# Kernel optimization log

Hardware: AMD Instinct MI355X
Metric: run time of the kernel (lower is better)

Reference implementation:

```python
import jax, jax.numpy as jnp
import numpy as np

D = 256  # subgraph_width
N_CLASSES = 10
EPS = 1e-5  # torch LayerNorm default


def _layernorm(x, g, b):
    mu = jnp.mean(x, axis=-1, keepdims=True)
    var = jnp.var(x, axis=-1, keepdims=True)
    return (x - mu) * jax.lax.rsqrt(var + EPS) * g + b


def setup_inputs() -> dict:
    key = jax.random.key(0)
    ks = jax.random.split(key, 16)
    B, T, N = 64, 512, 512
    traj = jax.random.normal(ks[0], (B, T, 2), dtype=jnp.float32)
    labels = jax.random.randint(ks[1], (B,), 0, N_CLASSES)
    h = jax.random.normal(ks[2], (B, N, D), dtype=jnp.float32)
    valid_len = jnp.maximum(jax.random.randint(ks[3], (B,), 0, N), 1)
    s = 0.02
    params = dict(
        emb=jax.random.normal(ks[4], (N_CLASSES, D), dtype=jnp.float32) * s,
        w_mlp=jax.random.normal(ks[5], (2, D), dtype=jnp.float32) * s,
        b_mlp=jnp.zeros((D,), jnp.float32),
        ln_g=jnp.ones((D,), jnp.float32),
        ln_b=jnp.zeros((D,), jnp.float32),
        wq=jax.random.normal(ks[6], (D, D), dtype=jnp.float32) * s,
        bq=jnp.zeros((D,), jnp.float32),
        wk=jax.random.normal(ks[7], (D, D), dtype=jnp.float32) * s,
        bk=jnp.zeros((D,), jnp.float32),
        wv=jax.random.normal(ks[8], (D, D), dtype=jnp.float32) * s,
        bv=jnp.zeros((D,), jnp.float32),
        w_out=jax.random.normal(ks[9], (D, 1), dtype=jnp.float32) * s,
        b_out=jnp.zeros((1,), jnp.float32),
    )
    return dict(traj=traj, labels=labels, h=h, valid_len=valid_len, **params)


def reference(traj, labels, h, valid_len, emb, w_mlp, b_mlp, ln_g, ln_b,
              wq, bq, wk, bk, wv, bv, w_out, b_out):
    # MLP(in=2, out=D, activation='leaky'): Linear -> LayerNorm -> LeakyReLU
    x = jax.nn.leaky_relu(_layernorm(traj @ w_mlp + b_mlp, ln_g, ln_b))  # [B,T,D]
    le = emb[labels]                          # [B,D]
    x = x + le[:, None, :]                    # embed-add
    # SelfAttentionWithKeyFCLayer: Q from x, K/V from h, scaled, key-masked by valid_len
    q = x @ wq + bq                            # [B,T,D]
    k = h @ wk + bk                            # [B,N,D]
    v = h @ wv + bv                            # [B,N,D]
    scores = jnp.einsum('btd,bnd->btn', q, k) / jnp.sqrt(jnp.float32(D))
    N = h.shape[1]
    key_mask = jnp.arange(N)[None, :] < valid_len[:, None]          # [B,N]
    scores = jnp.where(key_mask[:, None, :], scores, jnp.float32(-1e9))
    attn = jax.nn.softmax(scores, axis=-1)
    enc = jnp.einsum('btn,bnd->btd', attn, v)  # [B,T,D]
    pooled = jnp.max(enc, axis=1) + le          # [B,D]
    return jax.nn.sigmoid(pooled @ w_out + b_out)  # [B,1]
```

## Files before the change

kernel.cpp:

```cpp
#include <hip/hip_runtime.h>
#include <math.h>

typedef float f32x4 __attribute__((ext_vector_type(4)));
typedef __bf16 bf16x8 __attribute__((ext_vector_type(8)));
typedef unsigned short u16x8 __attribute__((ext_vector_type(8)));
typedef unsigned short u16x4 __attribute__((ext_vector_type(4)));
typedef unsigned int u32x4 __attribute__((ext_vector_type(4)));

#define MFMA(a, b, c) __builtin_amdgcn_mfma_f32_16x16x32_bf16((a), (b), (c), 0, 0, 0)

static __device__ __forceinline__ unsigned short f2bf(float f) {
  unsigned u = __float_as_uint(f);
  u += 0x7FFFu + ((u >> 16) & 1u);
  return (unsigned short)(u >> 16);
}
static __device__ __forceinline__ float bf2f(unsigned short s) {
  return __uint_as_float(((unsigned)s) << 16);
}
static __device__ __forceinline__ unsigned pack2bf(float lo, float hi) {
  return (unsigned)f2bf(lo) | ((unsigned)f2bf(hi) << 16);
}

static __device__ __forceinline__ int swz512(int row, int col) {
  return row * 512 + (col ^ ((((row & 7) ^ (col >> 6)) & 7) << 4));
}
static __device__ __forceinline__ int swzV(int d, int col) {
  return d * 64 + (col ^ (((d >> 1) & 3) << 4));
}
static __device__ __forceinline__ int swzO(int d, int col) {
  return d * 256 + (col ^ ((((d & 7) ^ (col >> 7)) & 7) << 4));
}

__global__ __launch_bounds__(256) void setup(
    const float* __restrict__ w0m, const float* __restrict__ w1m, const float* __restrict__ w2m,
    unsigned short* __restrict__ t0m, unsigned short* __restrict__ t1m, unsigned short* __restrict__ t2m,
    const float* __restrict__ w_mlp, const float* __restrict__ b_mlp, float* __restrict__ lnsc,
    const int* __restrict__ vlen, int* __restrict__ tasktab) {
  int bid = blockIdx.x;
  int t = threadIdx.x;
  if (bid == 48) {
    float w0 = w_mlp[t], w1 = w_mlp[256 + t], bb = b_mlp[t];
    float v[9] = {w0, w1, bb, w0 * w0, w1 * w1, w0 * w1, w0 * bb, w1 * bb, bb * bb};
    __shared__ float red[4][9];
#pragma unroll
    for (int j = 0; j < 9; ++j) {
      float s = v[j];
#pragma unroll
      for (int off = 32; off >= 1; off >>= 1) s += __shfl_xor(s, off, 64);
      v[j] = s;
    }
    if ((t & 63) == 0)
      for (int j = 0; j < 9; ++j) red[t >> 6][j] = v[j];
    __syncthreads();
    if (t < 9) lnsc[t] = red[0][t] + red[1][t] + red[2][t] + red[3][t];
    return;
  }
  if (bid == 49) {
    __shared__ int srank[64];
    if (t < 64) {
      int vb = vlen[t], r = 0;
      for (int j = 0; j < 64; ++j) {
        int vj = vlen[j];
        r += (vj > vb) || (vj == vb && j < t);
      }
      srank[r] = t;
    }
    __syncthreads();
    if (t < 64) {
      int r = t, b = srank[r];
      int xcd = r & 7, a = r >> 3;
      for (int tt = 0; tt < 4; ++tt)
        tasktab[(a * 4 + tt) * 8 + xcd] = (b << 2) | tt;
    }
    return;
  }
  int m = bid >> 4, t16 = bid & 15;
  const float* w = (m == 0) ? w0m : (m == 1) ? w1m : w2m;
  unsigned short* o = (m == 0) ? t0m : (m == 1) ? t1m : t2m;
  __shared__ float sm[64][65];
  int bi = t16 >> 2, bj = t16 & 3;
  for (int kb = 0; kb < 16; ++kb) {
    int idx = kb * 256 + t;
    int r = idx >> 6, c = idx & 63;
    sm[r][c] = w[(bi * 64 + r) * 256 + bj * 64 + c];
  }
  __syncthreads();
  for (int kb = 0; kb < 16; ++kb) {
    int idx = kb * 256 + t;
    int r = idx >> 6, c = idx & 63;
    int d = bj * 64 + r, e = bi * 64 + c;
    o[(e >> 5) * 8192 + d * 32 + (e & 31)] = f2bf(sm[c][r]);
  }
}

static __device__ __forceinline__ void gemm_direct(
    const unsigned short* __restrict__ Bpk, const unsigned short* Alds,
    int w, int g, int c15, f32x4 (&acc)[4][4]) {
  const unsigned short* bp = Bpk + (w * 64 + c15) * 32 + 8 * g;
#pragma unroll
  for (int c = 0; c < 8; ++c) {
    bf16x8 bfv[4];
#pragma unroll
    for (int nt = 0; nt < 4; ++nt)
      bfv[nt] = *(const bf16x8*)(bp + c * 8192 + nt * 512);
    bf16x8 af[4];
#pragma unroll
    for (int at = 0; at < 4; ++at)
      af[at] = *(const bf16x8*)((char*)Alds + swz512(at * 16 + c15, c * 64 + 16 * g));
    __builtin_amdgcn_s_setprio(1);
#pragma unroll
    for (int at = 0; at < 4; ++at)
#pragma unroll
      for (int nt = 0; nt < 4; ++nt) acc[at][nt] = MFMA(af[at], bfv[nt], acc[at][nt]);
    __builtin_amdgcn_s_setprio(0);
  }
}

__global__ __launch_bounds__(256, 4) void gemms(
    const float* __restrict__ h, const int* __restrict__ vlen,
    const unsigned short* __restrict__ wkPk, const float* __restrict__ bk,
    const unsigned short* __restrict__ wvPk, const float* __restrict__ bv,
    unsigned short* __restrict__ kout, unsigned short* __restrict__ vT) {
  __shared__ unsigned short Alds[64 * 256];
  int tid = threadIdx.x, w = tid >> 6, lane = tid & 63, g = lane >> 4, c15 = lane & 15;
  int tile = blockIdx.x;
  int b = tile >> 3;
  int nbase = (tile & 7) * 64;
  if (nbase >= vlen[b]) return;
  f32x4 acc[4][4];
  {
    const float* hb = h + (size_t)tile * 16384;
    f32x4 ha[8], hc[8];
#pragma unroll
    for (int i = 0; i < 8; ++i) {
      ha[i] = *(const f32x4*)(hb + i * 2048 + tid * 8);
      hc[i] = *(const f32x4*)(hb + i * 2048 + tid * 8 + 4);
    }
#pragma unroll
    for (int i = 0; i < 8; ++i) {
      u16x8 pk;
#pragma unroll
      for (int j = 0; j < 4; ++j) { pk[j] = f2bf(ha[i][j]); pk[j + 4] = f2bf(hc[i][j]); }
      *(u16x8*)((char*)Alds + swz512(i * 8 + (tid >> 5), (tid & 31) * 16)) = pk;
    }
  }
#pragma unroll
  for (int a = 0; a < 4; ++a)
#pragma unroll
    for (int n = 0; n < 4; ++n) acc[a][n] = (f32x4){0.f, 0.f, 0.f, 0.f};
  __syncthreads();

  gemm_direct(wvPk, Alds, w, g, c15, acc);
#pragma unroll
  for (int at = 0; at < 4; ++at)
#pragma unroll
    for (int nt = 0; nt < 4; ++nt) {
      int col = w * 64 + nt * 16 + c15;
      float bb = bv[col];
      u16x4 o;
#pragma unroll
      for (int r = 0; r < 4; ++r) o[r] = f2bf(acc[at][nt][r] + bb);
      *(u16x4*)(vT + (size_t)b * 131072 + (size_t)col * 512 + nbase + at * 16 + 4 * g) = o;
    }

#pragma unroll
  for (int a = 0; a < 4; ++a)
#pragma unroll
    for (int n = 0; n < 4; ++n) acc[a][n] = (f32x4){0.f, 0.f, 0.f, 0.f};
  gemm_direct(wkPk, Alds, w, g, c15, acc);
  __syncthreads();
#pragma unroll
  for (int at = 0; at < 4; ++at)
#pragma unroll
    for (int nt = 0; nt < 4; ++nt) {
      int col = w * 64 + nt * 16 + c15;
      float bb = bk[col];
#pragma unroll
      for (int r = 0; r < 4; ++r)
        *(unsigned short*)((char*)Alds + swz512(at * 16 + 4 * g + r, col * 2)) =
            f2bf(acc[at][nt][r] + bb);
    }
  __syncthreads();
  {
    int row = tid >> 2;
    for (int i = 0; i < 8; ++i) {
      int colb = (tid & 3) * 128 + i * 16;
      u16x8 vv = *(const u16x8*)((char*)Alds + swz512(row, colb));
      *(u16x8*)(kout + (size_t)(tile * 64 + row) * 256 + colb / 2) = vv;
    }
  }
}

__global__ __launch_bounds__(512, 2) void attn(
    const float* __restrict__ traj, const int* __restrict__ labels,
    const float* __restrict__ emb, const float* __restrict__ w_mlp,
    const float* __restrict__ b_mlp, const float* __restrict__ ln_g,
    const float* __restrict__ ln_b, const float* __restrict__ lnsc,
    const unsigned short* __restrict__ wqPk, const float* __restrict__ bq,
    const unsigned short* __restrict__ k, const unsigned short* __restrict__ vT,
    const int* __restrict__ valid_len, const int* __restrict__ tasktab,
    float* __restrict__ partial) {
  __shared__ unsigned short buf[2][16384];

  int task = tasktab[blockIdx.x];
  int b = task >> 2, tt = task & 3;
  int tid = threadIdx.x, w = tid >> 6, lane = tid & 63, g = lane >> 4, c15 = lane & 15;
  int vl = valid_len[b];
  int nit = (vl + 31) >> 5;
  bool isA = (w < 4);
  int wq4 = w & 3;

  {
    int rrow = tid >> 5, cb = (tid & 31) * 8;
    int lab = labels[b];
    f32x4 wa0 = *(const f32x4*)(w_mlp + cb), wa1 = *(const f32x4*)(w_mlp + cb + 4);
    f32x4 wb0 = *(const f32x4*)(w_mlp + 256 + cb), wb1 = *(const f32x4*)(w_mlp + 256 + cb + 4);
    f32x4 bm0 = *(const f32x4*)(b_mlp + cb), bm1 = *(const f32x4*)(b_mlp + cb + 4);
    f32x4 g0 = *(const f32x4*)(ln_g + cb), g1 = *(const f32x4*)(ln_g + cb + 4);
    f32x4 lb0 = *(const f32x4*)(ln_b + cb), lb1 = *(const f32x4*)(ln_b + cb + 4);
    f32x4 le0 = *(const f32x4*)(emb + lab * 256 + cb), le1 = *(const f32x4*)(emb + lab * 256 + cb + 4);
    float s0 = lnsc[0], s1 = lnsc[1], s2 = lnsc[2], s3 = lnsc[3], s4 = lnsc[4],
          s5 = lnsc[5], s6 = lnsc[6], s7 = lnsc[7], s8 = lnsc[8];
#pragma unroll
    for (int i = 0; i < 8; ++i) {
      int row = i * 16 + rrow, grow = b * 512 + tt * 128 + row;
      float t0 = traj[grow * 2], t1 = traj[grow * 2 + 1];
      float mu = (t0 * s0 + t1 * s1 + s2) * (1.f / 256.f);
      float ea2 = (t0 * t0 * s3 + t1 * t1 * s4 + s8 +
                   2.f * (t0 * t1 * s5 + t0 * s6 + t1 * s7)) * (1.f / 256.f);
      float rstd = rsqrtf(ea2 - mu * mu + 1e-5f);
      u16x8 pk;
#pragma unroll
      for (int j = 0; j < 4; ++j) {
        float a0 = t0 * wa0[j] + t1 * wb0[j] + bm0[j];
        float y0 = (a0 - mu) * rstd * g0[j] + lb0[j];
        pk[j] = f2bf((y0 > 0.f ? y0 : 0.01f * y0) + le0[j]);
        float a1 = t0 * wa1[j] + t1 * wb1[j] + bm1[j];
        float y1 = (a1 - mu) * rstd * g1[j] + lb1[j];
        pk[j + 4] = f2bf((y1 > 0.f ? y1 : 0.01f * y1) + le1[j]);
      }
      *(u16x8*)((char*)buf + swz512(row, cb * 2)) = pk;
    }
  }
  __syncthreads();

  {
    f32x4 qacc[4][4];
#pragma unroll
    for (int a = 0; a < 4; ++a)
#pragma unroll
      for (int n = 0; n < 4; ++n) qacc[a][n] = (f32x4){0.f, 0.f, 0.f, 0.f};
    int rbase = (w >> 2) * 64;
    const unsigned short* bp = wqPk + (wq4 * 64 + c15) * 32 + 8 * g;
#pragma unroll
    for (int c = 0; c < 8; ++c) {
      bf16x8 bfv[4];
#pragma unroll
      for (int nt = 0; nt < 4; ++nt)
        bfv[nt] = *(const bf16x8*)(bp + c * 8192 + nt * 512);
      bf16x8 af[4];
#pragma unroll
      for (int at = 0; at < 4; ++at)
        af[at] = *(const bf16x8*)((char*)buf + swz512(rbase + at * 16 + c15, c * 64 + 16 * g));
      __builtin_amdgcn_s_setprio(1);
#pragma unroll
      for (int at = 0; at < 4; ++at)
#pragma unroll
        for (int nt = 0; nt < 4; ++nt) qacc[at][nt] = MFMA(af[at], bfv[nt], qacc[at][nt]);
      __builtin_amdgcn_s_setprio(0);
    }
    __syncthreads();
#pragma unroll
    for (int nt = 0; nt < 4; ++nt) {
      int col = wq4 * 64 + nt * 16 + c15;
      float bb = bq[col];
#pragma unroll
      for (int at = 0; at < 4; ++at)
#pragma unroll
        for (int r = 0; r < 4; ++r)
          *(unsigned short*)((char*)buf + swz512(rbase + at * 16 + 4 * g + r, col * 2)) =
              f2bf(qacc[at][nt][r] + bb);
    }
  }
  __syncthreads();
  bf16x8 qf[2][8];
  if (isA) {
#pragma unroll
    for (int qt = 0; qt < 2; ++qt)
#pragma unroll
      for (int kk = 0; kk < 8; ++kk)
        qf[qt][kk] = *(const bf16x8*)((char*)buf + swz512(qt * 64 + wq4 * 16 + c15, kk * 64 + 16 * g));
  }
  __syncthreads();

  f32x4 acco[2][16];
#pragma unroll
  for (int qt = 0; qt < 2; ++qt)
#pragma unroll
    for (int i = 0; i < 16; ++i) acco[qt][i] = (f32x4){0.f, 0.f, 0.f, 0.f};
  float rs[2] = {0.f, 0.f};

  const unsigned short* kbase = k + (size_t)b * 512 * 256;
  const unsigned short* vbase = vT + (size_t)b * 131072;
  int t2 = tid & 255;

  if (!isA) {
    u16x8 kp[4], vp[4];
#pragma unroll
    for (int i = 0; i < 4; ++i) {
      int idx = t2 + 256 * i, key = idx >> 5, s = idx & 31;
      kp[i] = *(const u16x8*)(kbase + (size_t)key * 256 + s * 8);
    }
#pragma unroll
    for (int i = 0; i < 4; ++i) {
      int idx = t2 + 256 * i, d = idx >> 2, s = idx & 3;
      vp[i] = *(const u16x8*)(vbase + (size_t)d * 512 + s * 8);
    }
#pragma unroll
    for (int i = 0; i < 4; ++i) {
      int idx = t2 + 256 * i, key = idx >> 5, s = idx & 31;
      *(u16x8*)((char*)buf[0] + swz512(key, s * 16)) = kp[i];
    }
#pragma unroll
    for (int i = 0; i < 4; ++i) {
      int idx = t2 + 256 * i, d = idx >> 2, s = idx & 3;
      *(u16x8*)((char*)(buf[0] + 8192) + swzV(d, s * 16)) = vp[i];
    }
  }

  for (int it = 0; it < nit; ++it) {
    __syncthreads();
    if (isA) {
      const unsigned short* Klds = buf[it & 1];
      const unsigned short* Vlds = buf[it & 1] + 8192;
      int n0 = it * 32;
      f32x4 s4[2][2];
#pragma unroll
      for (int qt = 0; qt < 2; ++qt)
#pragma unroll
        for (int c = 0; c < 2; ++c) s4[qt][c] = (f32x4){0.f, 0.f, 0.f, 0.f};
      __builtin_amdgcn_s_setprio(1);
#pragma unroll
      for (int c = 0; c < 2; ++c)
#pragma unroll
        for (int kk = 0; kk < 8; ++kk) {
          bf16x8 kf = *(const bf16x8*)((char*)Klds + swz512(c * 16 + c15, kk * 64 + 16 * g));
          s4[0][c] = MFMA(kf, qf[0][kk], s4[0][c]);
          s4[1][c] = MFMA(kf, qf[1][kk], s4[1][c]);
        }
      __builtin_amdgcn_s_setprio(0);
      unsigned u01[2][2], u23[2][2];
#pragma unroll
      for (int qt = 0; qt < 2; ++qt)
#pragma unroll
        for (int c = 0; c < 2; ++c) {
          float p4[4];
#pragma unroll
          for (int r = 0; r < 4; ++r) {
            int key = n0 + c * 16 + 4 * g + r;
            float pv = (key < vl) ? __expf(s4[qt][c][r] * 0.0625f) : 0.f;
            p4[r] = pv;
            rs[qt] += pv;
          }
          u01[qt][c] = pack2bf(p4[0], p4[1]);
          u23[qt][c] = pack2bf(p4[2], p4[3]);
        }
      int srcA = c15 | ((lane & 16) << 1);
      int srcB = srcA + 16;
      bool hi = g >= 2;
      union { u32x4 u; bf16x8 v; } pa[2];
#pragma unroll
      for (int qt = 0; qt < 2; ++qt) {
        unsigned x0a = (unsigned)__shfl((int)u01[qt][0], srcA, 64);
        unsigned x1a = (unsigned)__shfl((int)u01[qt][1], srcA, 64);
        unsigned x0b = (unsigned)__shfl((int)u23[qt][0], srcA, 64);
        unsigned x1b = (unsigned)__shfl((int)u23[qt][1], srcA, 64);
        unsigned x0c = (unsigned)__shfl((int)u01[qt][0], srcB, 64);
        unsigned x1c = (unsigned)__shfl((int)u01[qt][1], srcB, 64);
        unsigned x0d = (unsigned)__shfl((int)u23[qt][0], srcB, 64);
        unsigned x1d = (unsigned)__shfl((int)u23[qt][1], srcB, 64);
        pa[qt].u[0] = hi ? x1a : x0a;
        pa[qt].u[1] = hi ? x1b : x0b;
        pa[qt].u[2] = hi ? x1c : x0c;
        pa[qt].u[3] = hi ? x1d : x0d;
      }
      __builtin_amdgcn_s_setprio(1);
#pragma unroll
      for (int dt = 0; dt < 16; ++dt) {
        bf16x8 vf = *(const bf16x8*)((char*)Vlds + swzV(dt * 16 + c15, 16 * g));
        acco[0][dt] = MFMA(vf, pa[0].v, acco[0][dt]);
        acco[1][dt] = MFMA(vf, pa[1].v, acco[1][dt]);
      }
      __builtin_amdgcn_s_setprio(0);
    } else if (it + 1 < nit) {
      int n1 = (it + 1) * 32;
      unsigned short* Kn = buf[(it + 1) & 1];
      unsigned short* Vn = buf[(it + 1) & 1] + 8192;
      u16x8 kp[4], vp[4];
#pragma unroll
      for (int i = 0; i < 4; ++i) {
        int idx = t2 + 256 * i, key = idx >> 5, s = idx & 31;
        kp[i] = *(const u16x8*)(kbase + (size_t)(n1 + key) * 256 + s * 8);
      }
#pragma unroll
      for (int i = 0; i < 4; ++i) {
        int idx = t2 + 256 * i, d = idx >> 2, s = idx & 3;
        vp[i] = *(const u16x8*)(vbase + (size_t)d * 512 + n1 + s * 8);
      }
#pragma unroll
      for (int i = 0; i < 4; ++i) {
        int idx = t2 + 256 * i, key = idx >> 5, s = idx & 31;
        *(u16x8*)((char*)Kn + swz512(key, s * 16)) = kp[i];
      }
#pragma unroll
      for (int i = 0; i < 4; ++i) {
        int idx = t2 + 256 * i, d = idx >> 2, s = idx & 3;
        *(u16x8*)((char*)Vn + swzV(d, s * 16)) = vp[i];
      }
    }
  }

  float inv[2];
  if (isA) {
#pragma unroll
    for (int qt = 0; qt < 2; ++qt) {
      rs[qt] += __shfl_xor(rs[qt], 16, 64);
      rs[qt] += __shfl_xor(rs[qt], 32, 64);
      inv[qt] = 1.f / rs[qt];
    }
  }
  __syncthreads();
  if (isA) {
#pragma unroll
    for (int qt = 0; qt < 2; ++qt) {
      int qcol = qt * 64 + wq4 * 16 + c15;
#pragma unroll
      for (int dt = 0; dt < 16; ++dt)
#pragma unroll
        for (int r = 0; r < 4; ++r) {
          int d = dt * 16 + 4 * g + r;
          *(unsigned short*)((char*)buf + swzO(d, qcol * 2)) = f2bf(acco[qt][dt][r] * inv[qt]);
        }
    }
  }
  __syncthreads();
  {
    int d = tid & 255, half = tid >> 8;
    float m = -1e30f;
    for (int i = 0; i < 8; ++i) {
      u16x8 vv = *(const u16x8*)((char*)buf + swzO(d, half * 128 + i * 16));
#pragma unroll
      for (int j = 0; j < 8; ++j) m = fmaxf(m, bf2f(vv[j]));
    }
    partial[(((size_t)b * 4 + tt) * 2 + half) * 256 + d] = m;
  }
}

__global__ __launch_bounds__(256) void finalize(
    const float* __restrict__ partial, const float* __restrict__ emb,
    const int* __restrict__ labels, const float* __restrict__ w_out,
    const float* __restrict__ b_out, float* __restrict__ out) {
  int b = blockIdx.x, t = threadIdx.x;
  float m = -1e30f;
#pragma unroll
  for (int s8 = 0; s8 < 8; ++s8)
    m = fmaxf(m, partial[((size_t)b * 8 + s8) * 256 + t]);
  m += emb[labels[b] * 256 + t];
  __shared__ float red[256];
  red[t] = m * w_out[t];
  __syncthreads();
  for (int s = 128; s > 0; s >>= 1) {
    if (t < s) red[t] += red[t + s];
    __syncthreads();
  }
  if (t == 0) out[b] = 1.f / (1.f + __expf(-(red[0] + b_out[0])));
}

extern "C" void kernel_launch(void* const* d_in, const int* in_sizes, int n_in,
                              void* d_out, int out_size, void* d_ws, size_t ws_size,
                              hipStream_t stream) {
  const float* traj   = (const float*)d_in[0];
  const int*   labels = (const int*)d_in[1];
  const float* h      = (const float*)d_in[2];
  const int*   vlen   = (const int*)d_in[3];
  const float* emb    = (const float*)d_in[4];
  const float* w_mlp  = (const float*)d_in[5];
  const float* b_mlp  = (const float*)d_in[6];
  const float* ln_g   = (const float*)d_in[7];
  const float* ln_b   = (const float*)d_in[8];
  const float* wq     = (const float*)d_in[9];
  const float* bq     = (const float*)d_in[10];
  const float* wk     = (const float*)d_in[11];
  const float* bk     = (const float*)d_in[12];
  const float* wv     = (const float*)d_in[13];
  const float* bv     = (const float*)d_in[14];
  const float* w_out  = (const float*)d_in[15];
  const float* b_out  = (const float*)d_in[16];
  float* out = (float*)d_out;

  unsigned short* kb   = (unsigned short*)d_ws;
  unsigned short* vT   = kb + (size_t)32768 * 256;
  unsigned short* wqPk = vT + (size_t)32768 * 256;
  unsigned short* wkPk = wqPk + 65536;
  unsigned short* wvPk = wkPk + 65536;
  float* lnsc    = (float*)(wvPk + 65536);
  float* partial = lnsc + 16;
  int*   tasktab = (int*)(partial + 64 * 8 * 256);

  setup<<<50, 256, 0, stream>>>(wq, wk, wv, wqPk, wkPk, wvPk, w_mlp, b_mlp, lnsc,
                                vlen, tasktab);
  gemms<<<512, 256, 0, stream>>>(h, vlen, wkPk, bk, wvPk, bv, kb, vT);
  attn<<<256, 512, 0, stream>>>(traj, labels, emb, w_mlp, b_mlp, ln_g, ln_b, lnsc,
                                wqPk, bq, kb, vT, vlen, tasktab, partial);
  finalize<<<64, 256, 0, stream>>>(partial, emb, labels, w_out, b_out, out);
}
```

Measured before the change: 79.06 us.

## Split attention into 64-row tasks and run K/V gemms on separate waves

Result: slower. 112.5 us (+42.3%).

```diff
diff --git a/kernel.cpp b/kernel.cpp
--- a/kernel.cpp
+++ b/kernel.cpp
@@ -27,8 +27,8 @@
 static __device__ __forceinline__ int swzV(int d, int col) {
   return d * 64 + (col ^ (((d >> 1) & 3) << 4));
 }
-static __device__ __forceinline__ int swzO(int d, int col) {
-  return d * 256 + (col ^ ((((d & 7) ^ (col >> 7)) & 7) << 4));
+static __device__ __forceinline__ int swzO64(int d, int col) {
+  return d * 128 + (col ^ ((d & 7) << 4));
 }
 
 __global__ __launch_bounds__(256) void setup(
@@ -69,8 +69,8 @@
     if (t < 64) {
       int r = t, b = srank[r];
       int xcd = r & 7, a = r >> 3;
-      for (int tt = 0; tt < 4; ++tt)
-        tasktab[(a * 4 + tt) * 8 + xcd] = (b << 2) | tt;
+      for (int tt = 0; tt < 8; ++tt)
+        tasktab[(a * 8 + tt) * 8 + xcd] = (b << 3) | tt;
     }
     return;
   }
@@ -116,12 +116,13 @@
   }
 }
 
-__global__ __launch_bounds__(256, 4) void gemms(
+__global__ __launch_bounds__(512, 4) void gemms(
     const float* __restrict__ h, const int* __restrict__ vlen,
     const unsigned short* __restrict__ wkPk, const float* __restrict__ bk,
     const unsigned short* __restrict__ wvPk, const float* __restrict__ bv,
     unsigned short* __restrict__ kout, unsigned short* __restrict__ vT) {
   __shared__ unsigned short Alds[64 * 256];
+  __shared__ unsigned short Klds[64 * 256];
   int tid = threadIdx.x, w = tid >> 6, lane = tid & 63, g = lane >> 4, c15 = lane & 15;
   int tile = blockIdx.x;
   int b = tile >> 3;
@@ -130,18 +131,18 @@
   f32x4 acc[4][4];
   {
     const float* hb = h + (size_t)tile * 16384;
-    f32x4 ha[8], hc[8];
-#pragma unroll
-    for (int i = 0; i < 8; ++i) {
-      ha[i] = *(const f32x4*)(hb + i * 2048 + tid * 8);
-      hc[i] = *(const f32x4*)(hb + i * 2048 + tid * 8 + 4);
-    }
-#pragma unroll
-    for (int i = 0; i < 8; ++i) {
+    f32x4 ha[4], hc[4];
+#pragma unroll
+    for (int i = 0; i < 4; ++i) {
+      ha[i] = *(const f32x4*)(hb + i * 4096 + tid * 8);
+      hc[i] = *(const f32x4*)(hb + i * 4096 + tid * 8 + 4);
+    }
+#pragma unroll
+    for (int i = 0; i < 4; ++i) {
       u16x8 pk;
 #pragma unroll
       for (int j = 0; j < 4; ++j) { pk[j] = f2bf(ha[i][j]); pk[j + 4] = f2bf(hc[i][j]); }
-      *(u16x8*)((char*)Alds + swz512(i * 8 + (tid >> 5), (tid & 31) * 16)) = pk;
+      *(u16x8*)((char*)Alds + swz512(i * 16 + (tid >> 5), (tid & 31) * 16)) = pk;
     }
   }
 #pragma unroll
@@ -150,48 +151,46 @@
     for (int n = 0; n < 4; ++n) acc[a][n] = (f32x4){0.f, 0.f, 0.f, 0.f};
   __syncthreads();
 
-  gemm_direct(wvPk, Alds, w, g, c15, acc);
-#pragma unroll
-  for (int at = 0; at < 4; ++at)
-#pragma unroll
-    for (int nt = 0; nt < 4; ++nt) {
-      int col = w * 64 + nt * 16 + c15;
-      float bb = bv[col];
-      u16x4 o;
-#pragma unroll
-      for (int r = 0; r < 4; ++r) o[r] = f2bf(acc[at][nt][r] + bb);
-      *(u16x4*)(vT + (size_t)b * 131072 + (size_t)col * 512 + nbase + at * 16 + 4 * g) = o;
-    }
-
-#pragma unroll
-  for (int a = 0; a < 4; ++a)
-#pragma unroll
-    for (int n = 0; n < 4; ++n) acc[a][n] = (f32x4){0.f, 0.f, 0.f, 0.f};
-  gemm_direct(wkPk, Alds, w, g, c15, acc);
-  __syncthreads();
-#pragma unroll
-  for (int at = 0; at < 4; ++at)
-#pragma unroll
-    for (int nt = 0; nt < 4; ++nt) {
-      int col = w * 64 + nt * 16 + c15;
-      float bb = bk[col];
-#pragma unroll
-      for (int r = 0; r < 4; ++r)
-        *(unsigned short*)((char*)Alds + swz512(at * 16 + 4 * g + r, col * 2)) =
-            f2bf(acc[at][nt][r] + bb);
-    }
-  __syncthreads();
-  {
+  int w4 = w & 3;
+  if (w < 4) {
+    gemm_direct(wvPk, Alds, w4, g, c15, acc);
+#pragma unroll
+    for (int at = 0; at < 4; ++at)
+#pragma unroll
+      for (int nt = 0; nt < 4; ++nt) {
+        int col = w4 * 64 + nt * 16 + c15;
+        float bb = bv[col];
+        u16x4 o;
+#pragma unroll
+        for (int r = 0; r < 4; ++r) o[r] = f2bf(acc[at][nt][r] + bb);
+        *(u16x4*)(vT + (size_t)b * 131072 + (size_t)col * 512 + nbase + at * 16 + 4 * g) = o;
+      }
+  } else {
+    gemm_direct(wkPk, Alds, w4, g, c15, acc);
+#pragma unroll
+    for (int at = 0; at < 4; ++at)
+#pragma unroll
+      for (int nt = 0; nt < 4; ++nt) {
+        int col = w4 * 64 + nt * 16 + c15;
+        float bb = bk[col];
+#pragma unroll
+        for (int r = 0; r < 4; ++r)
+          *(unsigned short*)((char*)Klds + swz512(at * 16 + 4 * g + r, col * 2)) =
+              f2bf(acc[at][nt][r] + bb);
+      }
+  }
+  __syncthreads();
+  if (tid < 256) {
     int row = tid >> 2;
     for (int i = 0; i < 8; ++i) {
       int colb = (tid & 3) * 128 + i * 16;
-      u16x8 vv = *(const u16x8*)((char*)Alds + swz512(row, colb));
+      u16x8 vv = *(const u16x8*)((char*)Klds + swz512(row, colb));
       *(u16x8*)(kout + (size_t)(tile * 64 + row) * 256 + colb / 2) = vv;
     }
   }
 }
 
-__global__ __launch_bounds__(512, 2) void attn(
+__global__ __launch_bounds__(256, 2) void attn(
     const float* __restrict__ traj, const int* __restrict__ labels,
     const float* __restrict__ emb, const float* __restrict__ w_mlp,
     const float* __restrict__ b_mlp, const float* __restrict__ ln_g,
@@ -200,15 +199,16 @@
     const unsigned short* __restrict__ k, const unsigned short* __restrict__ vT,
     const int* __restrict__ valid_len, const int* __restrict__ tasktab,
     float* __restrict__ partial) {
-  __shared__ unsigned short buf[2][16384];
+  __shared__ unsigned short ring[2][16384];
 
   int task = tasktab[blockIdx.x];
-  int b = task >> 2, tt = task & 3;
+  int b = task >> 3, tt = task & 7;
   int tid = threadIdx.x, w = tid >> 6, lane = tid & 63, g = lane >> 4, c15 = lane & 15;
   int vl = valid_len[b];
   int nit = (vl + 31) >> 5;
-  bool isA = (w < 4);
-  int wq4 = w & 3;
+  bool isA = (w < 2);
+  int cw = w & 1;
+  int tp = tid & 127;
 
   {
     int rrow = tid >> 5, cb = (tid & 31) * 8;
@@ -219,14 +219,14 @@
     f32x4 g0 = *(const f32x4*)(ln_g + cb), g1 = *(const f32x4*)(ln_g + cb + 4);
     f32x4 lb0 = *(const f32x4*)(ln_b + cb), lb1 = *(const f32x4*)(ln_b + cb + 4);
     f32x4 le0 = *(const f32x4*)(emb + lab * 256 + cb), le1 = *(const f32x4*)(emb + lab * 256 + cb + 4);
-    float s0 = lnsc[0], s1 = lnsc[1], s2 = lnsc[2], s3 = lnsc[3], s4 = lnsc[4],
+    float s0 = lnsc[0], s1 = lnsc[1], s2 = lnsc[2], s3 = lnsc[3], s4_ = lnsc[4],
           s5 = lnsc[5], s6 = lnsc[6], s7 = lnsc[7], s8 = lnsc[8];
 #pragma unroll
     for (int i = 0; i < 8; ++i) {
-      int row = i * 16 + rrow, grow = b * 512 + tt * 128 + row;
+      int row = i * 8 + rrow, grow = b * 512 + tt * 64 + row;
       float t0 = traj[grow * 2], t1 = traj[grow * 2 + 1];
       float mu = (t0 * s0 + t1 * s1 + s2) * (1.f / 256.f);
-      float ea2 = (t0 * t0 * s3 + t1 * t1 * s4 + s8 +
+      float ea2 = (t0 * t0 * s3 + t1 * t1 * s4_ + s8 +
                    2.f * (t0 * t1 * s5 + t0 * s6 + t1 * s7)) * (1.f / 256.f);
       float rstd = rsqrtf(ea2 - mu * mu + 1e-5f);
       u16x8 pk;
@@ -239,7 +239,7 @@
         float y1 = (a1 - mu) * rstd * g1[j] + lb1[j];
         pk[j + 4] = f2bf((y1 > 0.f ? y1 : 0.01f * y1) + le1[j]);
       }
-      *(u16x8*)((char*)buf + swz512(row, cb * 2)) = pk;
+      *(u16x8*)((char*)ring + swz512(row, cb * 2)) = pk;
     }
   }
   __syncthreads();
@@ -250,89 +250,72 @@
     for (int a = 0; a < 4; ++a)
 #pragma unroll
       for (int n = 0; n < 4; ++n) qacc[a][n] = (f32x4){0.f, 0.f, 0.f, 0.f};
-    int rbase = (w >> 2) * 64;
-    const unsigned short* bp = wqPk + (wq4 * 64 + c15) * 32 + 8 * g;
-#pragma unroll
-    for (int c = 0; c < 8; ++c) {
-      bf16x8 bfv[4];
-#pragma unroll
-      for (int nt = 0; nt < 4; ++nt)
-        bfv[nt] = *(const bf16x8*)(bp + c * 8192 + nt * 512);
-      bf16x8 af[4];
+    gemm_direct(wqPk, (const unsigned short*)ring, w, g, c15, qacc);
+#pragma unroll
+    for (int nt = 0; nt < 4; ++nt) {
+      int col = w * 64 + nt * 16 + c15;
+      float bb = bq[col];
 #pragma unroll
       for (int at = 0; at < 4; ++at)
-        af[at] = *(const bf16x8*)((char*)buf + swz512(rbase + at * 16 + c15, c * 64 + 16 * g));
-      __builtin_amdgcn_s_setprio(1);
-#pragma unroll
-      for (int at = 0; at < 4; ++at)
-#pragma unroll
-        for (int nt = 0; nt < 4; ++nt) qacc[at][nt] = MFMA(af[at], bfv[nt], qacc[at][nt]);
-      __builtin_amdgcn_s_setprio(0);
-    }
-    __syncthreads();
-#pragma unroll
-    for (int nt = 0; nt < 4; ++nt) {
-      int col = wq4 * 64 + nt * 16 + c15;
-      float bb = bq[col];
-#pragma unroll
-      for (int at = 0; at < 4; ++at)
 #pragma unroll
         for (int r = 0; r < 4; ++r)
-          *(unsigned short*)((char*)buf + swz512(rbase + at * 16 + 4 * g + r, col * 2)) =
+          *(unsigned short*)((char*)ring + 32768 + swz512(at * 16 + 4 * g + r, col * 2)) =
               f2bf(qacc[at][nt][r] + bb);
     }
   }
   __syncthreads();
+
+  f32x4 acco[2][16];
+#pragma unroll
+  for (int qt = 0; qt < 2; ++qt)
+#pragma unroll
+    for (int i = 0; i < 16; ++i) acco[qt][i] = (f32x4){0.f, 0.f, 0.f, 0.f};
+  float rs[2] = {0.f, 0.f};
+
+  const unsigned short* kbase = k + (size_t)b * 512 * 256;
+  const unsigned short* vbase = vT + (size_t)b * 131072;
+
+  auto STAGE = [&](int slot, int n0) {
+    char* base = (char*)ring + slot * 32768;
+    u16x8 kp[8], vp[8];
+#pragma unroll
+    for (int i = 0; i < 8; ++i) {
+      int idx = tp + 128 * i, key = idx >> 5, s = idx & 31;
+      kp[i] = *(const u16x8*)(kbase + (size_t)(n0 + key) * 256 + s * 8);
+    }
+#pragma unroll
+    for (int i = 0; i < 8; ++i) {
+      int idx = tp + 128 * i, d = idx >> 2, s = idx & 3;
+      vp[i] = *(const u16x8*)(vbase + (size_t)d * 512 + n0 + s * 8);
+    }
+#pragma unroll
+    for (int i = 0; i < 8; ++i) {
+      int idx = tp + 128 * i, key = idx >> 5, s = idx & 31;
+      *(u16x8*)(base + swz512(key, s * 16)) = kp[i];
+    }
+#pragma unroll
+    for (int i = 0; i < 8; ++i) {
+      int idx = tp + 128 * i, d = idx >> 2, s = idx & 3;
+      *(u16x8*)(base + 16384 + swzV(d, s * 16)) = vp[i];
+    }
+  };
+
   bf16x8 qf[2][8];
   if (isA) {
 #pragma unroll
     for (int qt = 0; qt < 2; ++qt)
 #pragma unroll
       for (int kk = 0; kk < 8; ++kk)
-        qf[qt][kk] = *(const bf16x8*)((char*)buf + swz512(qt * 64 + wq4 * 16 + c15, kk * 64 + 16 * g));
-  }
-  __syncthreads();
-
-  f32x4 acco[2][16];
-#pragma unroll
-  for (int qt = 0; qt < 2; ++qt)
-#pragma unroll
-    for (int i = 0; i < 16; ++i) acco[qt][i] = (f32x4){0.f, 0.f, 0.f, 0.f};
-  float rs[2] = {0.f, 0.f};
-
-  const unsigned short* kbase = k + (size_t)b * 512 * 256;
-  const unsigned short* vbase = vT + (size_t)b * 131072;
-  int t2 = tid & 255;
-
-  if (!isA) {
-    u16x8 kp[4], vp[4];
-#pragma unroll
-    for (int i = 0; i < 4; ++i) {
-      int idx = t2 + 256 * i, key = idx >> 5, s = idx & 31;
-      kp[i] = *(const u16x8*)(kbase + (size_t)key * 256 + s * 8);
-    }
-#pragma unroll
-    for (int i = 0; i < 4; ++i) {
-      int idx = t2 + 256 * i, d = idx >> 2, s = idx & 3;
-      vp[i] = *(const u16x8*)(vbase + (size_t)d * 512 + s * 8);
-    }
-#pragma unroll
-    for (int i = 0; i < 4; ++i) {
-      int idx = t2 + 256 * i, key = idx >> 5, s = idx & 31;
-      *(u16x8*)((char*)buf[0] + swz512(key, s * 16)) = kp[i];
-    }
-#pragma unroll
-    for (int i = 0; i < 4; ++i) {
-      int idx = t2 + 256 * i, d = idx >> 2, s = idx & 3;
-      *(u16x8*)((char*)(buf[0] + 8192) + swzV(d, s * 16)) = vp[i];
-    }
-  }
+        qf[qt][kk] = *(const bf16x8*)((char*)ring + 32768 +
+                                      swz512(cw * 32 + qt * 16 + c15, kk * 64 + 16 * g));
+  } else {
+    STAGE(0, 0);
+  }
+  __syncthreads();
 
   for (int it = 0; it < nit; ++it) {
-    __syncthreads();
     if (isA) {
-      const unsigned short* Klds = buf[it & 1];
-      const unsigned short* Vlds = buf[it & 1] + 8192;
+      const char* base = (const char*)ring + (it & 1) * 32768;
       int n0 = it * 32;
       f32x4 s4[2][2];
 #pragma unroll
@@ -344,7 +327,7 @@
       for (int c = 0; c < 2; ++c)
 #pragma unroll
         for (int kk = 0; kk < 8; ++kk) {
-          bf16x8 kf = *(const bf16x8*)((char*)Klds + swz512(c * 16 + c15, kk * 64 + 16 * g));
+          bf16x8 kf = *(const bf16x8*)(base + swz512(c * 16 + c15, kk * 64 + 16 * g));
           s4[0][c] = MFMA(kf, qf[0][kk], s4[0][c]);
           s4[1][c] = MFMA(kf, qf[1][kk], s4[1][c]);
         }
@@ -387,37 +370,15 @@
       __builtin_amdgcn_s_setprio(1);
 #pragma unroll
       for (int dt = 0; dt < 16; ++dt) {
-        bf16x8 vf = *(const bf16x8*)((char*)Vlds + swzV(dt * 16 + c15, 16 * g));
+        bf16x8 vf = *(const bf16x8*)(base + 16384 + swzV(dt * 16 + c15, 16 * g));
         acco[0][dt] = MFMA(vf, pa[0].v, acco[0][dt]);
         acco[1][dt] = MFMA(vf, pa[1].v, acco[1][dt]);
       }
       __builtin_amdgcn_s_setprio(0);
     } else if (it + 1 < nit) {
-      int n1 = (it + 1) * 32;
-      unsigned short* Kn = buf[(it + 1) & 1];
-      unsigned short* Vn = buf[(it + 1) & 1] + 8192;
-      u16x8 kp[4], vp[4];
-#pragma unroll
-      for (int i = 0; i < 4; ++i) {
-        int idx = t2 + 256 * i, key = idx >> 5, s = idx & 31;
-        kp[i] = *(const u16x8*)(kbase + (size_t)(n1 + key) * 256 + s * 8);
-      }
-#pragma unroll
-      for (int i = 0; i < 4; ++i) {
-        int idx = t2 + 256 * i, d = idx >> 2, s = idx & 3;
-        vp[i] = *(const u16x8*)(vbase + (size_t)d * 512 + n1 + s * 8);
-      }
-#pragma unroll
-      for (int i = 0; i < 4; ++i) {
-        int idx = t2 + 256 * i, key = idx >> 5, s = idx & 31;
-        *(u16x8*)((char*)Kn + swz512(key, s * 16)) = kp[i];
-      }
-#pragma unroll
-      for (int i = 0; i < 4; ++i) {
-        int idx = t2 + 256 * i, d = idx >> 2, s = idx & 3;
-        *(u16x8*)((char*)Vn + swzV(d, s * 16)) = vp[i];
-      }
-    }
+      STAGE((it + 1) & 1, (it + 1) * 32);
+    }
+    __syncthreads();
   }
 
   float inv[2];
@@ -428,31 +389,28 @@
       rs[qt] += __shfl_xor(rs[qt], 32, 64);
       inv[qt] = 1.f / rs[qt];
     }
-  }
-  __syncthreads();
-  if (isA) {
 #pragma unroll
     for (int qt = 0; qt < 2; ++qt) {
-      int qcol = qt * 64 + wq4 * 16 + c15;
+      int qcol = cw * 32 + qt * 16 + c15;
 #pragma unroll
       for (int dt = 0; dt < 16; ++dt)
 #pragma unroll
         for (int r = 0; r < 4; ++r) {
           int d = dt * 16 + 4 * g + r;
-          *(unsigned short*)((char*)buf + swzO(d, qcol * 2)) = f2bf(acco[qt][dt][r] * inv[qt]);
+          *(unsigned short*)((char*)ring + swzO64(d, qcol * 2)) = f2bf(acco[qt][dt][r] * inv[qt]);
         }
     }
   }
   __syncthreads();
   {
-    int d = tid & 255, half = tid >> 8;
+    int d = tid;
     float m = -1e30f;
     for (int i = 0; i < 8; ++i) {
-      u16x8 vv = *(const u16x8*)((char*)buf + swzO(d, half * 128 + i * 16));
+      u16x8 vv = *(const u16x8*)((char*)ring + swzO64(d, i * 16));
 #pragma unroll
       for (int j = 0; j < 8; ++j) m = fmaxf(m, bf2f(vv[j]));
     }
-    partial[(((size_t)b * 4 + tt) * 2 + half) * 256 + d] = m;
+    partial[((size_t)b * 8 + tt) * 256 + d] = m;
   }
 }
 
@@ -509,8 +467,8 @@
 
   setup<<<50, 256, 0, stream>>>(wq, wk, wv, wqPk, wkPk, wvPk, w_mlp, b_mlp, lnsc,
                                 vlen, tasktab);
-  gemms<<<512, 256, 0, stream>>>(h, vlen, wkPk, bk, wvPk, bv, kb, vT);
-  attn<<<256, 512, 0, stream>>>(traj, labels, emb, w_mlp, b_mlp, ln_g, ln_b, lnsc,
+  gemms<<<512, 512, 0, stream>>>(h, vlen, wkPk, bk, wvPk, bv, kb, vT);
+  attn<<<512, 256, 0, stream>>>(traj, labels, emb, w_mlp, b_mlp, ln_g, ln_b, lnsc,
                                 wqPk, bq, kb, vT, vlen, tasktab, partial);
   finalize<<<64, 256, 0, stream>>>(partial, emb, labels, w_out, b_out, out);
 }
```
